# Optimization experiments

Measured on AMD Instinct MI355X. Metric: run time of the kernel, lower is better.

## Reference

```python
import jax, jax.numpy as jnp
import numpy as np

SIZE = (2, 2)

def setup_inputs() -> dict:
    key = jax.random.key(0)
    k1, k2 = jax.random.split(key)
    B, H, W, C = 16, 128, 128, 64
    OH, OW = H * SIZE[0], W * SIZE[1]
    updates = jax.random.normal(k1, (B, H, W, C), dtype=jnp.float32)
    argmax = jax.random.randint(k2, (B, H, W, C), 0, OH * OW * C, dtype=jnp.int32)
    return {"updates": updates, "argmax": argmax}

def reference(updates, argmax):
    # Max-unpooling: scatter pooled values into an upsampled map at argmax positions.
    B, H, W, C = updates.shape
    OH, OW = H * SIZE[0], W * SIZE[1]
    # Decode flattened argmax (TF convention: ((y*OW + x)*C + c)) -> (y, x).
    y = (argmax // (OW * C)) % OH            # [B,H,W,C]
    x = (argmax // C) % OW                   # [B,H,W,C]
    # Batch and channel indices come from position, matching the TF code
    # (channel is taken from a tiled arange, NOT argmax % C).
    b = jnp.arange(B, dtype=jnp.int32).reshape(B, 1, 1, 1)
    c = jnp.arange(C, dtype=jnp.int32).reshape(1, 1, 1, C)
    out = jnp.zeros((B, OH, OW, C), dtype=updates.dtype)
    # tf.scatter_nd sums duplicate indices -> use .add
    out = out.at[b, y, x, c].add(updates)
    return out
```

## Files before the change

### kernel.cpp

```cpp
#include <hip/hip_runtime.h>


#define C_      64
#define N_ELEM  (16 * 128 * 128 * 64)
#define NB      1024
#define ST      512
#define CHE     8192
#define NBIN    512
#define NGB     8192
#define REGION  8192
#define PADCAP  (CHE + NBIN)

typedef int          i32x4 __attribute__((ext_vector_type(4)));
typedef float        f32x4 __attribute__((ext_vector_type(4)));
typedef unsigned int u32x2 __attribute__((ext_vector_type(2)));

__device__ __forceinline__ unsigned int f2bf(float f) {
    unsigned int u = __float_as_uint(f);
    return (u + 0x7fffu + ((u >> 16) & 1u)) >> 16;
}

__global__ __launch_bounds__(ST) void scatter_sort_kernel(
        const float* __restrict__ upd, const int* __restrict__ amx,
        unsigned int* __restrict__ pairs, int* __restrict__ lofs) {
    __shared__ unsigned int staging[PADCAP];
    __shared__ int h[NBIN];
    __shared__ int wsc[17];

    int t = threadIdx.x, lane = t & 63, w = t >> 6;
    int blk = blockIdx.x;
    int cc = (t & 15) << 2;

    const i32x4* amx4 = (const i32x4*)amx;
    const f32x4* upd4 = (const f32x4*)upd;

    int base4 = blk * 4096;
    i32x4 a[4]; f32x4 u[4];
    #pragma unroll
    for (int q = 0; q < 4; ++q) {
        a[q] = __builtin_nontemporal_load(amx4 + base4 + q * ST + t);
        u[q] = __builtin_nontemporal_load(upd4 + base4 + q * ST + t);
    }

    #pragma unroll
    for (int ch = 0; ch < 2; ++ch) {
        int bins[16]; unsigned int prs[16];
        #pragma unroll
        for (int q = 0; q < 4; ++q) {
            bins[4*q+0] = (a[q].x >> 13) & 511;
            prs [4*q+0] = (((unsigned)(a[q].x & 0x1FC0) | cc)       << 16) | f2bf(u[q].x);
            bins[4*q+1] = (a[q].y >> 13) & 511;
            prs [4*q+1] = (((unsigned)(a[q].y & 0x1FC0) | (cc + 1)) << 16) | f2bf(u[q].y);
            bins[4*q+2] = (a[q].z >> 13) & 511;
            prs [4*q+2] = (((unsigned)(a[q].z & 0x1FC0) | (cc + 2)) << 16) | f2bf(u[q].z);
            bins[4*q+3] = (a[q].w >> 13) & 511;
            prs [4*q+3] = (((unsigned)(a[q].w & 0x1FC0) | (cc + 3)) << 16) | f2bf(u[q].w);
        }
        if (ch == 0) {
            #pragma unroll
            for (int q = 0; q < 4; ++q) {
                a[q] = __builtin_nontemporal_load(amx4 + base4 + 2048 + q * ST + t);
                u[q] = __builtin_nontemporal_load(upd4 + base4 + 2048 + q * ST + t);
            }
        }

        h[t] = 0;
        __syncthreads();
        #pragma unroll
        for (int j = 0; j < 16; ++j) atomicAdd(&h[bins[j]], 1);
        __syncthreads();

        int cnt = h[t];
        int pcnt = (cnt + 1) & ~1;
        int incl = pcnt;
        #pragma unroll
        for (int off = 1; off < 64; off <<= 1) {
            int nv = __shfl_up(incl, off, 64);
            if (lane >= off) incl += nv;
        }
        if (lane == 63) wsc[w] = incl;
        __syncthreads();
        if (t < 8) {
            int s = 0;
            for (int j = 0; j < t; ++j) s += wsc[j];
            wsc[8 + t] = s;
        }
        __syncthreads();
        int excl = incl - pcnt + wsc[8 + w];
        h[t] = excl;
        int row = (2 * blk + ch) * 513;
        lofs[row + t] = excl;
        if (t == 511) {
            lofs[row + 512] = excl + pcnt;
            wsc[16] = excl + pcnt;
        }
        __syncthreads();

        if (cnt & 1) staging[excl + cnt] = 0u;
        #pragma unroll
        for (int j = 0; j < 16; ++j) {
            int slot = atomicAdd(&h[bins[j]], 1);
            staging[slot] = prs[j];
        }
        __syncthreads();

        int padM = wsc[16];
        uint4* dst = (uint4*)(pairs + (size_t)(2 * blk + ch) * PADCAP);
        int n4v = (padM + 3) >> 2;
        for (int k = t; k < n4v; k += ST)
            dst[k] = make_uint4(staging[4*k], staging[4*k+1],
                                staging[4*k+2], staging[4*k+3]);
        __syncthreads();
    }
}

__global__ __launch_bounds__(ST) void gather_accum_kernel(
        const unsigned int* __restrict__ pairs, const int* __restrict__ lofs,
        float* __restrict__ out) {
    __shared__ float acc[REGION];
    int g = blockIdx.x, t = threadIdx.x;
    int b = g >> 9, bin = g & 511;

    int seg = t >> 2, l4 = t & 3;
    int row = (b * 128 + seg) * 513 + bin;
    int s = lofs[row];
    int e = lofs[row + 1];
    int cnt2 = (e - s) >> 1;
    const u32x2* base2 = (const u32x2*)pairs
        + (((size_t)(b * 128 + seg) * PADCAP + s) >> 1);

    #pragma unroll
    for (int q = 0; q < 4; ++q)
        *(float4*)&acc[(q * ST + t) * 4] = make_float4(0.f, 0.f, 0.f, 0.f);
    __syncthreads();

    for (int i = l4; i < cnt2; i += 4) {
        u32x2 p = __builtin_nontemporal_load(base2 + i);
        atomicAdd(&acc[p.x >> 16], __uint_as_float(p.x << 16));
        atomicAdd(&acc[p.y >> 16], __uint_as_float(p.y << 16));
    }
    __syncthreads();

    f32x4* dst = (f32x4*)out + (size_t)g * (REGION / 4);
    #pragma unroll
    for (int q = 0; q < 4; ++q) {
        int k = q * ST + t;
        f32x4 v;
        v.x = acc[4*k]; v.y = acc[4*k+1]; v.z = acc[4*k+2]; v.w = acc[4*k+3];
        __builtin_nontemporal_store(v, dst + k);
    }
}

__global__ void zero_out_kernel(float4* __restrict__ out, int n4) {
    int stride = gridDim.x * blockDim.x;
    for (int i = blockIdx.x * blockDim.x + threadIdx.x; i < n4; i += stride)
        out[i] = make_float4(0.f, 0.f, 0.f, 0.f);
}

__global__ void unpool_atomic_kernel(const float4* __restrict__ upd4,
                                     const int4* __restrict__ amx4,
                                     float* __restrict__ out, int n4) {
    int i = blockIdx.x * blockDim.x + threadIdx.x;
    if (i >= n4) return;
    float4 u = upd4[i];
    int4   a = amx4[i];
    int e = i << 2;
    int c = e & (C_ - 1);
    int base_b = (e >> 20) << 22;
    int y, x;
    y = (a.x >> 14) & 255; x = (a.x >> 6) & 255;
    atomicAdd(&out[base_b + (y << 14) + (x << 6) + c], u.x);
    y = (a.y >> 14) & 255; x = (a.y >> 6) & 255;
    atomicAdd(&out[base_b + (y << 14) + (x << 6) + c + 1], u.y);
    y = (a.z >> 14) & 255; x = (a.z >> 6) & 255;
    atomicAdd(&out[base_b + (y << 14) + (x << 6) + c + 2], u.z);
    y = (a.w >> 14) & 255; x = (a.w >> 6) & 255;
    atomicAdd(&out[base_b + (y << 14) + (x << 6) + c + 3], u.w);
}

extern "C" void kernel_launch(void* const* d_in, const int* in_sizes, int n_in,
                              void* d_out, int out_size, void* d_ws, size_t ws_size,
                              hipStream_t stream) {
    const float* updates = (const float*)d_in[0];
    const int*   argmax  = (const int*)d_in[1];

    size_t pair_bytes = (size_t)NB * 2 * PADCAP * 4;
    size_t lofs_bytes = (size_t)NB * 2 * 513 * 4;
    size_t need = pair_bytes + lofs_bytes;

    if (in_sizes[0] == N_ELEM && ws_size >= need) {
        char* ws = (char*)d_ws;
        unsigned int* pairs = (unsigned int*)ws;
        int*          lofs  = (int*)(ws + pair_bytes);

        scatter_sort_kernel<<<NB, ST, 0, stream>>>(
            updates, argmax, pairs, lofs);
        gather_accum_kernel<<<NGB, ST, 0, stream>>>(pairs, lofs, (float*)d_out);
    } else {
        int n_out4 = out_size >> 2;
        zero_out_kernel<<<2048, 256, 0, stream>>>((float4*)d_out, n_out4);
        int n4 = in_sizes[0] >> 2;
        unpool_atomic_kernel<<<(n4 + 255) / 256, 256, 0, stream>>>(
            (const float4*)updates, (const int4*)argmax, (float*)d_out, n4);
    }
}
```

Measured before the change: 151.6 us.

## Process two output regions per gather block with double LDS accumulators

The gather kernel now runs 1024 threads per block and handles two adjacent output regions, each in its own LDS accumulator. Eight lanes per source segment replace four. The write-out of region A is placed before the accumulation of region B so that stores can overlap with the second region's loads and atomics. In exchange it uses twice the LDS per block, which lowers the number of resident blocks, and it halves the grid size.

```diff
diff --git a/kernel.cpp b/kernel.cpp
--- a/kernel.cpp
+++ b/kernel.cpp
@@ -5,9 +5,10 @@
 #define N_ELEM  (16 * 128 * 128 * 64)
 #define NB      1024
 #define ST      512
+#define GT      1024
 #define CHE     8192
 #define NBIN    512
-#define NGB     8192
+#define NGB     4096
 #define REGION  8192
 #define PADCAP  (CHE + NBIN)
 
@@ -114,40 +115,63 @@
     }
 }
 
-__global__ __launch_bounds__(ST) void gather_accum_kernel(
+__global__ __launch_bounds__(GT) void gather_accum_kernel(
         const unsigned int* __restrict__ pairs, const int* __restrict__ lofs,
         float* __restrict__ out) {
-    __shared__ float acc[REGION];
-    int g = blockIdx.x, t = threadIdx.x;
-    int b = g >> 9, bin = g & 511;
-
-    int seg = t >> 2, l4 = t & 3;
-    int row = (b * 128 + seg) * 513 + bin;
-    int s = lofs[row];
-    int e = lofs[row + 1];
-    int cnt2 = (e - s) >> 1;
-    const u32x2* base2 = (const u32x2*)pairs
-        + (((size_t)(b * 128 + seg) * PADCAP + s) >> 1);
-
-    #pragma unroll
-    for (int q = 0; q < 4; ++q)
-        *(float4*)&acc[(q * ST + t) * 4] = make_float4(0.f, 0.f, 0.f, 0.f);
+    __shared__ float accA[REGION];
+    __shared__ float accB[REGION];
+    int t = threadIdx.x;
+    int gA = 2 * blockIdx.x, gB = gA + 1;
+    int bA = gA >> 9, binA = gA & 511;
+    int bB = gB >> 9, binB = gB & 511;
+
+    int seg = t >> 3, l8 = t & 7;
+    int rowA = (bA * 128 + seg) * 513 + binA;
+    int rowB = (bB * 128 + seg) * 513 + binB;
+    int sA = lofs[rowA], eA = lofs[rowA + 1];
+    int sB = lofs[rowB], eB = lofs[rowB + 1];
+    int cntA = (eA - sA) >> 1, cntB = (eB - sB) >> 1;
+    const u32x2* baseA = (const u32x2*)pairs
+        + (((size_t)(bA * 128 + seg) * PADCAP + sA) >> 1);
+    const u32x2* baseB = (const u32x2*)pairs
+        + (((size_t)(bB * 128 + seg) * PADCAP + sB) >> 1);
+
+    #pragma unroll
+    for (int q = 0; q < 2; ++q) {
+        *(float4*)&accA[(q * GT + t) * 4] = make_float4(0.f, 0.f, 0.f, 0.f);
+        *(float4*)&accB[(q * GT + t) * 4] = make_float4(0.f, 0.f, 0.f, 0.f);
+    }
     __syncthreads();
 
-    for (int i = l4; i < cnt2; i += 4) {
-        u32x2 p = __builtin_nontemporal_load(base2 + i);
-        atomicAdd(&acc[p.x >> 16], __uint_as_float(p.x << 16));
-        atomicAdd(&acc[p.y >> 16], __uint_as_float(p.y << 16));
+    for (int i = l8; i < cntA; i += 8) {
+        u32x2 p = __builtin_nontemporal_load(baseA + i);
+        atomicAdd(&accA[p.x >> 16], __uint_as_float(p.x << 16));
+        atomicAdd(&accA[p.y >> 16], __uint_as_float(p.y << 16));
     }
     __syncthreads();
 
-    f32x4* dst = (f32x4*)out + (size_t)g * (REGION / 4);
-    #pragma unroll
-    for (int q = 0; q < 4; ++q) {
-        int k = q * ST + t;
+    f32x4* dstA = (f32x4*)out + (size_t)gA * (REGION / 4);
+    #pragma unroll
+    for (int q = 0; q < 2; ++q) {
+        int k = q * GT + t;
         f32x4 v;
-        v.x = acc[4*k]; v.y = acc[4*k+1]; v.z = acc[4*k+2]; v.w = acc[4*k+3];
-        __builtin_nontemporal_store(v, dst + k);
+        v.x = accA[4*k]; v.y = accA[4*k+1]; v.z = accA[4*k+2]; v.w = accA[4*k+3];
+        __builtin_nontemporal_store(v, dstA + k);
+    }
+    for (int i = l8; i < cntB; i += 8) {
+        u32x2 p = __builtin_nontemporal_load(baseB + i);
+        atomicAdd(&accB[p.x >> 16], __uint_as_float(p.x << 16));
+        atomicAdd(&accB[p.y >> 16], __uint_as_float(p.y << 16));
+    }
+    __syncthreads();
+
+    f32x4* dstB = (f32x4*)out + (size_t)gB * (REGION / 4);
+    #pragma unroll
+    for (int q = 0; q < 2; ++q) {
+        int k = q * GT + t;
+        f32x4 v;
+        v.x = accB[4*k]; v.y = accB[4*k+1]; v.z = accB[4*k+2]; v.w = accB[4*k+3];
+        __builtin_nontemporal_store(v, dstB + k);
     }
 }
 
@@ -195,7 +219,7 @@
 
         scatter_sort_kernel<<<NB, ST, 0, stream>>>(
             updates, argmax, pairs, lofs);
-        gather_accum_kernel<<<NGB, ST, 0, stream>>>(pairs, lofs, (float*)d_out);
+        gather_accum_kernel<<<NGB, GT, 0, stream>>>(pairs, lofs, (float*)d_out);
     } else {
         int n_out4 = out_size >> 2;
         zero_out_kernel<<<2048, 256, 0, stream>>>((float4*)d_out, n_out4);
```

New measurement: 158.8 us. 4.8% more time.
